# Kernel tuning notes

Measured on AMD Instinct MI355X. Metric: run time of the kernel, lower is better.

Reference implementation:

```python
import jax, jax.numpy as jnp
import numpy as np

B, N, S = 4, 8192, 2048
C1, C2 = 128, 256
CIN = C1 + C2  # 384
H1, H2 = 256, 256
BN_EPS = 1e-5


def setup_inputs() -> dict:
    key = jax.random.key(0)
    ks = jax.random.split(key, 12)
    inp = {
        "xyz1": jax.random.normal(ks[0], (B, N, 3), jnp.float32),
        "xyz2": jax.random.normal(ks[1], (B, S, 3), jnp.float32),
        "points1": jax.random.normal(ks[2], (B, C1, N), jnp.float32),
        "points2": jax.random.normal(ks[3], (B, C2, S), jnp.float32),
        # Conv1d(k=1) weights are [out, in]; BN affine params per channel
        "W1": jax.random.normal(ks[4], (H1, CIN), jnp.float32) * (1.0 / np.sqrt(CIN)),
        "b1": jnp.zeros((H1,), jnp.float32),
        "gamma1": jnp.ones((H1,), jnp.float32),
        "beta1": jnp.zeros((H1,), jnp.float32),
        "W2": jax.random.normal(ks[5], (H2, H1), jnp.float32) * (1.0 / np.sqrt(H1)),
        "b2": jnp.zeros((H2,), jnp.float32),
        "gamma2": jnp.ones((H2,), jnp.float32),
        "beta2": jnp.zeros((H2,), jnp.float32),
    }
    return inp


def _square_distance(src, dst):
    # src [B,N,3], dst [B,S,3] -> [B,N,S]
    d = -2.0 * jnp.einsum("bnc,bsc->bns", src, dst)
    d = d + jnp.sum(src * src, -1)[:, :, None]
    d = d + jnp.sum(dst * dst, -1)[:, None, :]
    return jnp.maximum(d, 0.0)


def _bn_relu(x, gamma, beta):
    # x [B,C,N]; BatchNorm1d in training mode: batch stats over (B, N), biased var
    mean = jnp.mean(x, axis=(0, 2), keepdims=True)
    var = jnp.mean((x - mean) ** 2, axis=(0, 2), keepdims=True)
    xhat = (x - mean) * jax.lax.rsqrt(var + BN_EPS)
    return jax.nn.relu(xhat * gamma[None, :, None] + beta[None, :, None])


def reference(xyz1, xyz2, points1, points2, W1, b1, gamma1, beta1, W2, b2, gamma2, beta2):
    dists = _square_distance(xyz1, xyz2)            # [B,N,S]
    neg_d, idx = jax.lax.top_k(-dists, 3)           # 3 smallest distances
    d3 = -neg_d                                     # [B,N,3]
    recip = 1.0 / (d3 + 1e-8)
    weight = recip / jnp.sum(recip, axis=2, keepdims=True)  # [B,N,3]
    pts2 = jnp.transpose(points2, (0, 2, 1))        # [B,S,C2]
    gathered = jax.vmap(lambda p, i: p[i])(pts2, idx)  # [B,N,3,C2]
    interp = jnp.einsum("bnkc,bnk->bcn", gathered, weight)  # [B,C2,N]
    new_pts = jnp.concatenate([points1, interp], axis=1)    # [B,CIN,N]
    x = jnp.einsum("oc,bcn->bon", W1, new_pts) + b1[None, :, None]
    x = _bn_relu(x, gamma1, beta1)
    x = jnp.einsum("oc,bcn->bon", W2, x) + b2[None, :, None]
    x = _bn_relu(x, gamma2, beta2)
    return x
```

## Files before the change

### kernel.cpp

```cpp
#include <hip/hip_runtime.h>

#define B_   4
#define N_   8192
#define S_   2048
#define C1_  128
#define C2_  256
#define CIN_ 384
#define H_   256

typedef short short8 __attribute__((ext_vector_type(8)));
typedef unsigned short ushort8 __attribute__((ext_vector_type(8)));
typedef float f32x4 __attribute__((ext_vector_type(4)));

__device__ __forceinline__ unsigned short f2bf(float x) {
  unsigned u = __float_as_uint(x);
  unsigned r = (u + 0x7fffu + ((u >> 16) & 1u)) >> 16;
  return (unsigned short)r;
}
__device__ __forceinline__ float bf2f(unsigned short h) {
  return __uint_as_float(((unsigned)h) << 16);
}
__device__ __forceinline__ void async16(const void* g, void* l) {
  __builtin_amdgcn_global_load_lds(
      (const __attribute__((address_space(1))) void*)g,
      (__attribute__((address_space(3))) void*)l, 16, 0, 0);
}

__global__ __launch_bounds__(256) void convw_kernel(const float* __restrict__ W1,
                                                    const float* __restrict__ W2,
                                                    unsigned short* __restrict__ W1b,
                                                    unsigned short* __restrict__ W2b) {
  int id = blockIdx.x * 256 + threadIdx.x;
  if (id < 98304) W1b[id] = f2bf(W1[id]);
  else            W2b[id - 98304] = f2bf(W2[id - 98304]);
}

__global__ __launch_bounds__(256) void transpose_kernel(
    const float* __restrict__ src, unsigned short* __restrict__ dst,
    int dstStride) {
  __shared__ float tile[64 * 65];
  const int b = blockIdx.z;
  const int n0 = blockIdx.x * 64;
  const int c0 = blockIdx.y * 64;
  const int C = gridDim.y * 64;
  const int Nsrc = gridDim.x * 64;
  const int tid = threadIdx.x;
  const float* sp = src + ((size_t)b * C + c0) * Nsrc;
  unsigned short* dp = dst + (size_t)b * Nsrc * dstStride;
  const int c_l = tid >> 2, nch = (tid & 3) * 16;
  const float* s = sp + (size_t)c_l * Nsrc + n0 + nch;
#pragma unroll
  for (int i = 0; i < 4; ++i)
    *(float4*)&tile[c_l * 65 + nch + i * 4] = *(const float4*)(s + i * 4);
  __syncthreads();
  const int n_l = tid >> 2, cch = (tid & 3) * 16;
  unsigned short pk[16];
#pragma unroll
  for (int i = 0; i < 16; ++i) pk[i] = f2bf(tile[(cch + i) * 65 + n_l]);
  unsigned short* d = dp + (size_t)(n0 + n_l) * dstStride + c0 + cch;
  *(uint4*)d = *(uint4*)pk;
  *(uint4*)(d + 8) = *(uint4*)(pk + 8);
}

__global__ __launch_bounds__(512) void knn_kernel(const float* __restrict__ xyz1,
                                                  const float* __restrict__ xyz2,
                                                  int* __restrict__ idx,
                                                  float* __restrict__ wgt) {
  __shared__ float4 t4[S_];
  __shared__ float kd[64][25];
  __shared__ int   ki[64][25];
  const int b  = blockIdx.x >> 7;
  const int n0 = (blockIdx.x & 127) << 6;
  const int tid = threadIdx.x;

  for (int i = tid; i < S_; i += 512) {
    float x = xyz2[(b * S_ + i) * 3 + 0];
    float y = xyz2[(b * S_ + i) * 3 + 1];
    float z = xyz2[(b * S_ + i) * 3 + 2];
    t4[i] = make_float4(-2.f * x, -2.f * y, -2.f * z,
                        fmaf(x, x, fmaf(y, y, z * z)));
  }
  __syncthreads();

  const int w = tid >> 6;
  const int ln = tid & 63;
  const int n = n0 + ln;
  const float px = xyz1[(b * N_ + n) * 3 + 0];
  const float py = xyz1[(b * N_ + n) * 3 + 1];
  const float pz = xyz1[(b * N_ + n) * 3 + 2];
  const float h = fmaf(px, px, fmaf(py, py, pz * pz));

  float d0 = 1e30f, d1 = 1e30f, d2 = 1e30f;
  int j0 = 0, j1 = 0, j2 = 0;
  const int jg0 = w * 256;
  const float4* tp = t4 + jg0;
#pragma unroll 4
  for (int j = 0; j < 256; ++j) {
    float4 t = tp[j];
    float d = fmaf(px, t.x, fmaf(py, t.y, fmaf(pz, t.z, t.w))) + h;
    d = fmaxf(d, 0.f);
    const int jj = jg0 + j;
    bool c0 = d < d0, c1 = d < d1, c2 = d < d2;
    float nd2 = c1 ? d1 : (c2 ? d : d2);
    int   nj2 = c1 ? j1 : (c2 ? jj : j2);
    float nd1 = c0 ? d0 : (c1 ? d : d1);
    int   nj1 = c0 ? j0 : (c1 ? jj : j1);
    d0 = c0 ? d : d0;
    j0 = c0 ? jj : j0;
    d1 = nd1; j1 = nj1;
    d2 = nd2; j2 = nj2;
  }
  kd[ln][w * 3 + 0] = d0; ki[ln][w * 3 + 0] = j0;
  kd[ln][w * 3 + 1] = d1; ki[ln][w * 3 + 1] = j1;
  kd[ln][w * 3 + 2] = d2; ki[ln][w * 3 + 2] = j2;
  __syncthreads();

  if (tid < 64) {
    float m0 = kd[tid][0], m1 = kd[tid][1], m2 = kd[tid][2];
    int   i0 = ki[tid][0], i1 = ki[tid][1], i2 = ki[tid][2];
#pragma unroll
    for (int s = 3; s < 24; ++s) {
      float d = kd[tid][s];
      int  jj = ki[tid][s];
      bool c0 = d < m0, c1 = d < m1, c2 = d < m2;
      float nd2 = c1 ? m1 : (c2 ? d : m2);
      int   nj2 = c1 ? i1 : (c2 ? jj : i2);
      float nd1 = c0 ? m0 : (c1 ? d : m1);
      int   nj1 = c0 ? i0 : (c1 ? jj : i1);
      m0 = c0 ? d : m0;
      i0 = c0 ? jj : i0;
      m1 = nd1; i1 = nj1;
      m2 = nd2; i2 = nj2;
    }
    float r0 = 1.f / (m0 + 1e-8f);
    float r1 = 1.f / (m1 + 1e-8f);
    float r2 = 1.f / (m2 + 1e-8f);
    float rs = 1.f / (r0 + r1 + r2);
    int base = (b * N_ + n0 + tid) * 3;
    idx[base + 0] = i0;
    idx[base + 1] = i1;
    idx[base + 2] = i2;
    wgt[base + 0] = r0 * rs;
    wgt[base + 1] = r1 * rs;
    wgt[base + 2] = r2 * rs;
  }
}

__global__ __launch_bounds__(256) void interp_gather_kernel(
    const unsigned short* __restrict__ p2t, const int* __restrict__ idx,
    const float* __restrict__ wgt, unsigned short* __restrict__ Xt) {
  const int w = threadIdx.x >> 6, lane = threadIdx.x & 63;
  const int gbase = blockIdx.x * 128 + w * 32;
#pragma unroll 2
  for (int i = 0; i < 32; ++i) {
    const int gn = gbase + i;
    const int b = gn >> 13;
    const int base = gn * 3;
    int i0 = idx[base], i1 = idx[base + 1], i2 = idx[base + 2];
    float w0 = wgt[base], w1 = wgt[base + 1], w2 = wgt[base + 2];
    const unsigned short* r0 = p2t + (((size_t)(b * S_ + i0)) << 8) + lane * 4;
    const unsigned short* r1 = p2t + (((size_t)(b * S_ + i1)) << 8) + lane * 4;
    const unsigned short* r2 = p2t + (((size_t)(b * S_ + i2)) << 8) + lane * 4;
    uint2 a = *(const uint2*)r0;
    uint2 c = *(const uint2*)r1;
    uint2 e = *(const uint2*)r2;
    const unsigned short* ap = (const unsigned short*)&a;
    const unsigned short* cp = (const unsigned short*)&c;
    const unsigned short* ep = (const unsigned short*)&e;
    unsigned short pk[4];
#pragma unroll
    for (int k = 0; k < 4; ++k) {
      float v = w0 * bf2f(ap[k]) + w1 * bf2f(cp[k]) + w2 * bf2f(ep[k]);
      pk[k] = f2bf(v);
    }
    *(uint2*)(Xt + (size_t)gn * CIN_ + C1_ + lane * 4) = *(uint2*)pk;
  }
}

template <int K, bool FUSE>
__global__ __launch_bounds__(256, 2) void gemm_mfma_kernel(
    const unsigned short* __restrict__ Wb,
    const unsigned short* __restrict__ Bmat,
    const float* __restrict__ bias,
    const float* __restrict__ bnscale, const float* __restrict__ bnshift,
    float* __restrict__ OutF, unsigned short* __restrict__ OutB,
    float* __restrict__ Psum, float* __restrict__ Psq) {
  __shared__ __align__(16) short Als[128 * 32];
  __shared__ __align__(16) short Bls[128 * 32];
  const int tid = threadIdx.x;
  const int lane = tid & 63;
  const int col = lane & 15, quad = lane >> 4;
  const int wid = tid >> 6;
  const int wr = wid >> 1, wc = wid & 1;
  const int nBase = blockIdx.x * 128;
  const int oBase = blockIdx.y * 128;
  const int b = blockIdx.z;

  f32x4 acc[4][4];
#pragma unroll
  for (int i = 0; i < 4; ++i)
#pragma unroll
    for (int j = 0; j < 4; ++j) acc[i][j] = (f32x4){0.f, 0.f, 0.f, 0.f};

  const int f0 = tid * 16;
  const int m0 = f0 >> 6;
  const int kb0 = f0 & 63;
  const char* Abase = (const char*)Wb;
  const char* Bbase = (const char*)Bmat;
  char* AldsW = (char*)Als + (tid & ~63) * 16;
  char* BldsW = (char*)Bls + (tid & ~63) * 16;

  for (int k0 = 0; k0 < K; k0 += 32) {
    __syncthreads();
    async16(Abase + ((size_t)(oBase + m0) * K + k0) * 2 + kb0, AldsW);
    async16(Abase + ((size_t)(oBase + m0 + 64) * K + k0) * 2 + kb0, AldsW + 4096);
    if (!FUSE) {
      async16(Bbase + ((size_t)(b * N_ + nBase + m0) * K + k0) * 2 + kb0, BldsW);
      async16(Bbase + ((size_t)(b * N_ + nBase + m0 + 64) * K + k0) * 2 + kb0,
              BldsW + 4096);
    } else {
#pragma unroll
      for (int r = 0; r < 2; ++r) {
        const int f = f0 + r * 4096;
        const int n = f >> 6;
        const int kb = f & 63;
        const int ke = k0 + (kb >> 1);
        ushort8 h = *(const ushort8*)(Bbase +
            ((size_t)(b * N_ + nBase + n) * K + k0) * 2 + kb);
        float4 s0 = *(const float4*)(bnscale + ke);
        float4 s1 = *(const float4*)(bnscale + ke + 4);
        float4 t0 = *(const float4*)(bnshift + ke);
        float4 t1 = *(const float4*)(bnshift + ke + 4);
        float sc[8] = {s0.x, s0.y, s0.z, s0.w, s1.x, s1.y, s1.z, s1.w};
        float sh[8] = {t0.x, t0.y, t0.z, t0.w, t1.x, t1.y, t1.z, t1.w};
        unsigned short pk[8];
#pragma unroll
        for (int e = 0; e < 8; ++e)
          pk[e] = f2bf(fmaxf(fmaf(bf2f(h[e]), sc[e], sh[e]), 0.f));
        *(uint4*)((char*)Bls + f) = *(uint4*)pk;
      }
    }
    __syncthreads();
    short8 af[4], bfr[4];
#pragma unroll
    for (int i = 0; i < 4; ++i)
      af[i] = *(const short8*)(Als + (wr * 64 + i * 16 + col) * 32 + quad * 8);
#pragma unroll
    for (int j = 0; j < 4; ++j)
      bfr[j] = *(const short8*)(Bls + (wc * 64 + j * 16 + col) * 32 + quad * 8);
#pragma unroll
    for (int i = 0; i < 4; ++i)
#pragma unroll
      for (int j = 0; j < 4; ++j)
        acc[i][j] = __builtin_amdgcn_mfma_f32_16x16x32_bf16(af[i], bfr[j],
                                                            acc[i][j], 0, 0, 0);
  }

  float s_acc[4][4], q_acc[4][4];
#pragma unroll
  for (int i = 0; i < 4; ++i) {
    const int oloc = wr * 64 + i * 16 + quad * 4;
    float4 bb = *(const float4*)(bias + oBase + oloc);
    float s[4] = {0.f, 0.f, 0.f, 0.f}, q[4] = {0.f, 0.f, 0.f, 0.f};
#pragma unroll
    for (int j = 0; j < 4; ++j) {
      const int n = nBase + wc * 64 + j * 16 + col;
      float v0 = acc[i][j][0] + bb.x;
      float v1 = acc[i][j][1] + bb.y;
      float v2 = acc[i][j][2] + bb.z;
      float v3 = acc[i][j][3] + bb.w;
      if (!FUSE) {
        unsigned short pk[4] = {f2bf(v0), f2bf(v1), f2bf(v2), f2bf(v3)};
        *(uint2*)(OutB + (size_t)(b * N_ + n) * H_ + oBase + oloc) = *(uint2*)pk;
      } else {
        float* op = OutF + ((size_t)b * H_ + oBase + oloc) * N_ + n;
        op[0] = v0; op[N_] = v1; op[2 * N_] = v2; op[3 * N_] = v3;
      }
      s[0] += v0; q[0] = fmaf(v0, v0, q[0]);
      s[1] += v1; q[1] = fmaf(v1, v1, q[1]);
      s[2] += v2; q[2] = fmaf(v2, v2, q[2]);
      s[3] += v3; q[3] = fmaf(v3, v3, q[3]);
    }
#pragma unroll
    for (int reg = 0; reg < 4; ++reg) {
      float ss = s[reg], qq = q[reg];
#pragma unroll
      for (int m = 1; m < 16; m <<= 1) {
        ss += __shfl_xor(ss, m);
        qq += __shfl_xor(qq, m);
      }
      s_acc[i][reg] = ss;
      q_acc[i][reg] = qq;
    }
  }
  __syncthreads();
  float* red = (float*)Als;
#pragma unroll
  for (int i = 0; i < 4; ++i)
#pragma unroll
    for (int reg = 0; reg < 4; ++reg)
      if (col == 0) {
        int ch = wr * 64 + i * 16 + quad * 4 + reg;
        red[wc * 256 + ch] = s_acc[i][reg];
        red[wc * 256 + 128 + ch] = q_acc[i][reg];
      }
  __syncthreads();
  {
    const int wcb = tid >> 7, ch = tid & 127;
    const int part = (blockIdx.z * 64 + blockIdx.x) * 2 + wcb;
    Psum[part * 256 + oBase + ch] = red[wcb * 256 + ch];
    Psq[part * 256 + oBase + ch]  = red[wcb * 256 + 128 + ch];
  }
}

__global__ __launch_bounds__(1024) void finalize_bn_kernel(
    const float* __restrict__ Psum, const float* __restrict__ Psq,
    const float* __restrict__ gamma, const float* __restrict__ beta,
    float* __restrict__ scale, float* __restrict__ shift) {
  __shared__ float ls[4][2][256];
  const int tid = threadIdx.x;
  const int g = tid >> 8, ch = tid & 255;
  float s = 0.f, q = 0.f;
#pragma unroll 4
  for (int p = g * 128; p < (g + 1) * 128; ++p) {
    s += Psum[p * 256 + ch];
    q += Psq[p * 256 + ch];
  }
  ls[g][0][ch] = s;
  ls[g][1][ch] = q;
  __syncthreads();
  if (tid < 256) {
    float ss = ls[0][0][ch] + ls[1][0][ch] + ls[2][0][ch] + ls[3][0][ch];
    float qq = ls[0][1][ch] + ls[1][1][ch] + ls[2][1][ch] + ls[3][1][ch];
    const float inv_n = 1.f / 32768.f;
    float mean = ss * inv_n;
    float var = qq * inv_n - mean * mean;
    float sc = gamma[ch] * rsqrtf(var + 1e-5f);
    scale[ch] = sc;
    shift[ch] = fmaf(-mean, sc, beta[ch]);
  }
}

__global__ __launch_bounds__(256) void bn_apply_kernel(float* __restrict__ io,
                                                       const float* __restrict__ scale,
                                                       const float* __restrict__ shift) {
  int id = blockIdx.x * 256 + threadIdx.x;
  int row = id >> 11;
  int o = row & 255;
  float sc = scale[o], sh = shift[o];
  float4 v = ((float4*)io)[id];
  v.x = fmaxf(fmaf(v.x, sc, sh), 0.f);
  v.y = fmaxf(fmaf(v.y, sc, sh), 0.f);
  v.z = fmaxf(fmaf(v.z, sc, sh), 0.f);
  v.w = fmaxf(fmaf(v.w, sc, sh), 0.f);
  ((float4*)io)[id] = v;
}

extern "C" void kernel_launch(void* const* d_in, const int* in_sizes, int n_in,
                              void* d_out, int out_size, void* d_ws, size_t ws_size,
                              hipStream_t stream) {
  const float* xyz1 = (const float*)d_in[0];
  const float* xyz2 = (const float*)d_in[1];
  const float* p1   = (const float*)d_in[2];
  const float* p2   = (const float*)d_in[3];
  const float* W1   = (const float*)d_in[4];
  const float* b1   = (const float*)d_in[5];
  const float* g1   = (const float*)d_in[6];
  const float* be1  = (const float*)d_in[7];
  const float* W2   = (const float*)d_in[8];
  const float* b2   = (const float*)d_in[9];
  const float* g2   = (const float*)d_in[10];
  const float* be2  = (const float*)d_in[11];
  float* out = (float*)d_out;

  unsigned short* ws = (unsigned short*)d_ws;
  unsigned short* Xt  = ws;
  unsigned short* Y1t = Xt + 12582912;
  unsigned short* p2t = Y1t + 8388608;
  unsigned short* W1b = p2t + 2097152;
  unsigned short* W2b = W1b + 98304;
  float* wgt   = (float*)(W2b + 65536);
  int*   idxb  = (int*)(wgt + 98304);
  float* Psum1 = (float*)(idxb + 98304);
  float* Psq1  = Psum1 + 131072;
  float* Psum2 = Psq1 + 131072;
  float* Psq2  = Psum2 + 131072;
  float* scale1 = Psq2 + 131072;
  float* shift1 = scale1 + 256;
  float* scale2 = shift1 + 256;
  float* shift2 = scale2 + 256;

  convw_kernel<<<640, 256, 0, stream>>>(W1, W2, W1b, W2b);
  transpose_kernel<<<dim3(32, 4, 4), 256, 0, stream>>>(p2, p2t, C2_);
  knn_kernel<<<512, 512, 0, stream>>>(xyz1, xyz2, idxb, wgt);
  transpose_kernel<<<dim3(128, 2, 4), 256, 0, stream>>>(p1, Xt, CIN_);
  interp_gather_kernel<<<256, 256, 0, stream>>>(p2t, idxb, wgt, Xt);

  dim3 gg(64, 2, 4);
  gemm_mfma_kernel<CIN_, false><<<gg, 256, 0, stream>>>(
      W1b, Xt, b1, nullptr, nullptr, nullptr, Y1t, Psum1, Psq1);
  finalize_bn_kernel<<<1, 1024, 0, stream>>>(Psum1, Psq1, g1, be1, scale1, shift1);
  gemm_mfma_kernel<H_, true><<<gg, 256, 0, stream>>>(
      W2b, Y1t, b2, scale1, shift1, out, nullptr, Psum2, Psq2);
  finalize_bn_kernel<<<1, 1024, 0, stream>>>(Psum2, Psq2, g2, be2, scale2, shift2);
  bn_apply_kernel<<<8192, 256, 0, stream>>>(out, scale2, shift2);
}
```

Before: 220.6 us.

## Merge prep stages into one kernel and run GEMM/BN chain as cooperative megakernel

Converts weights, transposes both point feature tensors, and runs KNN inside a single block-partitioned prep kernel; the KNN part now uses 256-thread blocks scanning 512 candidates per wave. The interpolation gather, both GEMMs, BN statistics finalization and the final BN+ReLU run in one cooperative kernel with grid syncs, keeping the second GEMM's accumulators in registers so the output is written once instead of written then re-read by a separate apply pass. This targets launch overhead and the extra full-output round trip, at the cost of grid-wide barriers, finalize steps done by only 8 blocks while the rest idle, and a fallback path if cooperative launch fails.

```diff
diff --git a/kernel.cpp b/kernel.cpp
--- a/kernel.cpp
+++ b/kernel.cpp
@@ -1,4 +1,7 @@
 #include <hip/hip_runtime.h>
+#include <hip/hip_cooperative_groups.h>
+
+namespace cg = cooperative_groups;
 
 #define B_   4
 #define N_   8192
@@ -26,27 +29,21 @@
       (__attribute__((address_space(3))) void*)l, 16, 0, 0);
 }
 
-__global__ __launch_bounds__(256) void convw_kernel(const float* __restrict__ W1,
-                                                    const float* __restrict__ W2,
-                                                    unsigned short* __restrict__ W1b,
-                                                    unsigned short* __restrict__ W2b) {
-  int id = blockIdx.x * 256 + threadIdx.x;
-  if (id < 98304) W1b[id] = f2bf(W1[id]);
-  else            W2b[id - 98304] = f2bf(W2[id - 98304]);
-}
-
-__global__ __launch_bounds__(256) void transpose_kernel(
+union PrepShared {
+  struct {
+    float4 t4[S_];
+    float  kd[64][13];
+    int    ki[64][13];
+  } k;
+  float tile[64 * 65];
+};
+
+__device__ __forceinline__ void transpose_tile(
     const float* __restrict__ src, unsigned short* __restrict__ dst,
-    int dstStride) {
-  __shared__ float tile[64 * 65];
-  const int b = blockIdx.z;
-  const int n0 = blockIdx.x * 64;
-  const int c0 = blockIdx.y * 64;
-  const int C = gridDim.y * 64;
-  const int Nsrc = gridDim.x * 64;
-  const int tid = threadIdx.x;
-  const float* sp = src + ((size_t)b * C + c0) * Nsrc;
-  unsigned short* dp = dst + (size_t)b * Nsrc * dstStride;
+    float* tile, int x, int y, int z, int C, int Nsrc, int dstStride, int tid) {
+  const int n0 = x * 64, c0 = y * 64;
+  const float* sp = src + ((size_t)z * C + c0) * Nsrc;
+  unsigned short* dp = dst + (size_t)z * Nsrc * dstStride;
   const int c_l = tid >> 2, nch = (tid & 3) * 16;
   const float* s = sp + (size_t)c_l * Nsrc + n0 + nch;
 #pragma unroll
@@ -62,87 +59,109 @@
   *(uint4*)(d + 8) = *(uint4*)(pk + 8);
 }
 
-__global__ __launch_bounds__(512) void knn_kernel(const float* __restrict__ xyz1,
-                                                  const float* __restrict__ xyz2,
-                                                  int* __restrict__ idx,
-                                                  float* __restrict__ wgt) {
-  __shared__ float4 t4[S_];
-  __shared__ float kd[64][25];
-  __shared__ int   ki[64][25];
-  const int b  = blockIdx.x >> 7;
-  const int n0 = (blockIdx.x & 127) << 6;
-  const int tid = threadIdx.x;
-
-  for (int i = tid; i < S_; i += 512) {
-    float x = xyz2[(b * S_ + i) * 3 + 0];
-    float y = xyz2[(b * S_ + i) * 3 + 1];
-    float z = xyz2[(b * S_ + i) * 3 + 2];
-    t4[i] = make_float4(-2.f * x, -2.f * y, -2.f * z,
-                        fmaf(x, x, fmaf(y, y, z * z)));
-  }
-  __syncthreads();
-
-  const int w = tid >> 6;
-  const int ln = tid & 63;
-  const int n = n0 + ln;
-  const float px = xyz1[(b * N_ + n) * 3 + 0];
-  const float py = xyz1[(b * N_ + n) * 3 + 1];
-  const float pz = xyz1[(b * N_ + n) * 3 + 2];
-  const float h = fmaf(px, px, fmaf(py, py, pz * pz));
-
-  float d0 = 1e30f, d1 = 1e30f, d2 = 1e30f;
-  int j0 = 0, j1 = 0, j2 = 0;
-  const int jg0 = w * 256;
-  const float4* tp = t4 + jg0;
+__global__ __launch_bounds__(256) void prep_kernel(
+    const float* __restrict__ W1, const float* __restrict__ W2,
+    unsigned short* __restrict__ W1b, unsigned short* __restrict__ W2b,
+    const float* __restrict__ p1, const float* __restrict__ p2,
+    unsigned short* __restrict__ Xt, unsigned short* __restrict__ p2t,
+    const float* __restrict__ xyz1, const float* __restrict__ xyz2,
+    int* __restrict__ idx, float* __restrict__ wgt) {
+  __shared__ PrepShared sm;
+  const int blk = blockIdx.x, tid = threadIdx.x;
+
+  if (blk < 640) {
+    int id = blk * 256 + tid;
+    if (id < 98304) W1b[id] = f2bf(W1[id]);
+    else            W2b[id - 98304] = f2bf(W2[id - 98304]);
+    return;
+  }
+  if (blk < 1152) {
+    int t = blk - 640;
+    transpose_tile(p2, p2t, sm.tile, t & 31, (t >> 5) & 3, t >> 7,
+                   C2_, S_, C2_, tid);
+    return;
+  }
+  if (blk < 2176) {
+    int t = blk - 1152;
+    transpose_tile(p1, Xt, sm.tile, t & 127, (t >> 7) & 1, t >> 8,
+                   C1_, N_, CIN_, tid);
+    return;
+  }
+  {
+    const int t = blk - 2176;
+    const int b = t >> 7;
+    const int n0 = (t & 127) << 6;
+    for (int i = tid; i < S_; i += 256) {
+      float x = xyz2[(b * S_ + i) * 3 + 0];
+      float y = xyz2[(b * S_ + i) * 3 + 1];
+      float z = xyz2[(b * S_ + i) * 3 + 2];
+      sm.k.t4[i] = make_float4(-2.f * x, -2.f * y, -2.f * z,
+                               fmaf(x, x, fmaf(y, y, z * z)));
+    }
+    __syncthreads();
+
+    const int w = tid >> 6;
+    const int ln = tid & 63;
+    const int n = n0 + ln;
+    const float px = xyz1[(b * N_ + n) * 3 + 0];
+    const float py = xyz1[(b * N_ + n) * 3 + 1];
+    const float pz = xyz1[(b * N_ + n) * 3 + 2];
+    const float h = fmaf(px, px, fmaf(py, py, pz * pz));
+
+    float d0 = 1e30f, d1 = 1e30f, d2 = 1e30f;
+    int j0 = 0, j1 = 0, j2 = 0;
+    const int jg0 = w * 512;
+    const float4* tp = sm.k.t4 + jg0;
 #pragma unroll 4
-  for (int j = 0; j < 256; ++j) {
-    float4 t = tp[j];
-    float d = fmaf(px, t.x, fmaf(py, t.y, fmaf(pz, t.z, t.w))) + h;
-    d = fmaxf(d, 0.f);
-    const int jj = jg0 + j;
-    bool c0 = d < d0, c1 = d < d1, c2 = d < d2;
-    float nd2 = c1 ? d1 : (c2 ? d : d2);
-    int   nj2 = c1 ? j1 : (c2 ? jj : j2);
-    float nd1 = c0 ? d0 : (c1 ? d : d1);
-    int   nj1 = c0 ? j0 : (c1 ? jj : j1);
-    d0 = c0 ? d : d0;
-    j0 = c0 ? jj : j0;
-    d1 = nd1; j1 = nj1;
-    d2 = nd2; j2 = nj2;
-  }
-  kd[ln][w * 3 + 0] = d0; ki[ln][w * 3 + 0] = j0;
-  kd[ln][w * 3 + 1] = d1; ki[ln][w * 3 + 1] = j1;
-  kd[ln][w * 3 + 2] = d2; ki[ln][w * 3 + 2] = j2;
-  __syncthreads();
-
-  if (tid < 64) {
-    float m0 = kd[tid][0], m1 = kd[tid][1], m2 = kd[tid][2];
-    int   i0 = ki[tid][0], i1 = ki[tid][1], i2 = ki[tid][2];
-#pragma unroll
-    for (int s = 3; s < 24; ++s) {
-      float d = kd[tid][s];
-      int  jj = ki[tid][s];
-      bool c0 = d < m0, c1 = d < m1, c2 = d < m2;
-      float nd2 = c1 ? m1 : (c2 ? d : m2);
-      int   nj2 = c1 ? i1 : (c2 ? jj : i2);
-      float nd1 = c0 ? m0 : (c1 ? d : m1);
-      int   nj1 = c0 ? i0 : (c1 ? jj : i1);
-      m0 = c0 ? d : m0;
-      i0 = c0 ? jj : i0;
-      m1 = nd1; i1 = nj1;
-      m2 = nd2; i2 = nj2;
-    }
-    float r0 = 1.f / (m0 + 1e-8f);
-    float r1 = 1.f / (m1 + 1e-8f);
-    float r2 = 1.f / (m2 + 1e-8f);
-    float rs = 1.f / (r0 + r1 + r2);
-    int base = (b * N_ + n0 + tid) * 3;
-    idx[base + 0] = i0;
-    idx[base + 1] = i1;
-    idx[base + 2] = i2;
-    wgt[base + 0] = r0 * rs;
-    wgt[base + 1] = r1 * rs;
-    wgt[base + 2] = r2 * rs;
+    for (int j = 0; j < 512; ++j) {
+      float4 tt = tp[j];
+      float d = fmaf(px, tt.x, fmaf(py, tt.y, fmaf(pz, tt.z, tt.w))) + h;
+      d = fmaxf(d, 0.f);
+      const int jj = jg0 + j;
+      bool c0 = d < d0, c1 = d < d1, c2 = d < d2;
+      float nd2 = c1 ? d1 : (c2 ? d : d2);
+      int   nj2 = c1 ? j1 : (c2 ? jj : j2);
+      float nd1 = c0 ? d0 : (c1 ? d : d1);
+      int   nj1 = c0 ? j0 : (c1 ? jj : j1);
+      d0 = c0 ? d : d0;
+      j0 = c0 ? jj : j0;
+      d1 = nd1; j1 = nj1;
+      d2 = nd2; j2 = nj2;
+    }
+    sm.k.kd[ln][w * 3 + 0] = d0; sm.k.ki[ln][w * 3 + 0] = j0;
+    sm.k.kd[ln][w * 3 + 1] = d1; sm.k.ki[ln][w * 3 + 1] = j1;
+    sm.k.kd[ln][w * 3 + 2] = d2; sm.k.ki[ln][w * 3 + 2] = j2;
+    __syncthreads();
+
+    if (tid < 64) {
+      float m0 = sm.k.kd[tid][0], m1 = sm.k.kd[tid][1], m2 = sm.k.kd[tid][2];
+      int   i0 = sm.k.ki[tid][0], i1 = sm.k.ki[tid][1], i2 = sm.k.ki[tid][2];
+#pragma unroll
+      for (int s = 3; s < 12; ++s) {
+        float d = sm.k.kd[tid][s];
+        int  jj = sm.k.ki[tid][s];
+        bool c0 = d < m0, c1 = d < m1, c2 = d < m2;
+        float nd2 = c1 ? m1 : (c2 ? d : m2);
+        int   nj2 = c1 ? i1 : (c2 ? jj : i2);
+        float nd1 = c0 ? m0 : (c1 ? d : m1);
+        int   nj1 = c0 ? i0 : (c1 ? jj : i1);
+        m0 = c0 ? d : m0;
+        i0 = c0 ? jj : i0;
+        m1 = nd1; i1 = nj1;
+        m2 = nd2; i2 = nj2;
+      }
+      float r0 = 1.f / (m0 + 1e-8f);
+      float r1 = 1.f / (m1 + 1e-8f);
+      float r2 = 1.f / (m2 + 1e-8f);
+      float rs = 1.f / (r0 + r1 + r2);
+      int base = (b * N_ + n0 + tid) * 3;
+      idx[base + 0] = i0;
+      idx[base + 1] = i1;
+      idx[base + 2] = i2;
+      wgt[base + 0] = r0 * rs;
+      wgt[base + 1] = r1 * rs;
+      wgt[base + 2] = r2 * rs;
+    }
   }
 }
 
@@ -150,20 +169,17 @@
     const unsigned short* __restrict__ p2t, const int* __restrict__ idx,
     const float* __restrict__ wgt, unsigned short* __restrict__ Xt) {
   const int w = threadIdx.x >> 6, lane = threadIdx.x & 63;
-  const int gbase = blockIdx.x * 128 + w * 32;
+  const int gbase = blockIdx.x * 64 + w * 16;
 #pragma unroll 2
-  for (int i = 0; i < 32; ++i) {
+  for (int i = 0; i < 16; ++i) {
     const int gn = gbase + i;
     const int b = gn >> 13;
     const int base = gn * 3;
     int i0 = idx[base], i1 = idx[base + 1], i2 = idx[base + 2];
     float w0 = wgt[base], w1 = wgt[base + 1], w2 = wgt[base + 2];
-    const unsigned short* r0 = p2t + (((size_t)(b * S_ + i0)) << 8) + lane * 4;
-    const unsigned short* r1 = p2t + (((size_t)(b * S_ + i1)) << 8) + lane * 4;
-    const unsigned short* r2 = p2t + (((size_t)(b * S_ + i2)) << 8) + lane * 4;
-    uint2 a = *(const uint2*)r0;
-    uint2 c = *(const uint2*)r1;
-    uint2 e = *(const uint2*)r2;
+    uint2 a = *(const uint2*)(p2t + (((size_t)(b * S_ + i0)) << 8) + lane * 4);
+    uint2 c = *(const uint2*)(p2t + (((size_t)(b * S_ + i1)) << 8) + lane * 4);
+    uint2 e = *(const uint2*)(p2t + (((size_t)(b * S_ + i2)) << 8) + lane * 4);
     const unsigned short* ap = (const unsigned short*)&a;
     const unsigned short* cp = (const unsigned short*)&c;
     const unsigned short* ep = (const unsigned short*)&e;
@@ -356,6 +372,266 @@
   ((float4*)io)[id] = v;
 }
 
+struct MegaArgs {
+  const unsigned short* p2t;
+  const int* idx;
+  const float* wgt;
+  unsigned short* Xt;
+  const unsigned short* W1b;
+  const float *b1, *g1, *be1;
+  const unsigned short* W2b;
+  const float *b2, *g2, *be2;
+  unsigned short* Y1t;
+  float *Psum1, *Psq1, *Psum2, *Psq2;
+  float *scale1, *shift1, *scale2, *shift2;
+  float* out;
+};
+
+template <int K, bool FUSE, bool WRITE_OUT>
+__device__ __forceinline__ void gemm_phase(
+    const unsigned short* __restrict__ Wb,
+    const unsigned short* __restrict__ Bmat,
+    const float* __restrict__ bias,
+    const float* __restrict__ bnscale, const float* __restrict__ bnshift,
+    unsigned short* __restrict__ OutB,
+    float* __restrict__ Psum, float* __restrict__ Psq,
+    short* Als, short* Bls, f32x4 (&acc)[4][4],
+    const int tid, const int nBase, const int oBase, const int b,
+    const int part2) {
+  const int lane = tid & 63;
+  const int col = lane & 15, quad = lane >> 4;
+  const int wid = tid >> 6;
+  const int wr = wid >> 1, wc = wid & 1;
+
+#pragma unroll
+  for (int i = 0; i < 4; ++i)
+#pragma unroll
+    for (int j = 0; j < 4; ++j) acc[i][j] = (f32x4){0.f, 0.f, 0.f, 0.f};
+
+  const int f0 = tid * 16;
+  const int m0 = f0 >> 6;
+  const int kb0 = f0 & 63;
+  const char* Abase = (const char*)Wb;
+  const char* Bbase = (const char*)Bmat;
+  char* AldsW = (char*)Als + (tid & ~63) * 16;
+  char* BldsW = (char*)Bls + (tid & ~63) * 16;
+
+  for (int k0 = 0; k0 < K; k0 += 32) {
+    __syncthreads();
+    async16(Abase + ((size_t)(oBase + m0) * K + k0) * 2 + kb0, AldsW);
+    async16(Abase + ((size_t)(oBase + m0 + 64) * K + k0) * 2 + kb0, AldsW + 4096);
+    if (!FUSE) {
+      async16(Bbase + ((size_t)(b * N_ + nBase + m0) * K + k0) * 2 + kb0, BldsW);
+      async16(Bbase + ((size_t)(b * N_ + nBase + m0 + 64) * K + k0) * 2 + kb0,
+              BldsW + 4096);
+    } else {
+#pragma unroll
+      for (int r = 0; r < 2; ++r) {
+        const int f = f0 + r * 4096;
+        const int n = f >> 6;
+        const int kb = f & 63;
+        const int ke = k0 + (kb >> 1);
+        ushort8 h = *(const ushort8*)(Bbase +
+            ((size_t)(b * N_ + nBase + n) * K + k0) * 2 + kb);
+        float4 s0 = *(const float4*)(bnscale + ke);
+        float4 s1 = *(const float4*)(bnscale + ke + 4);
+        float4 t0 = *(const float4*)(bnshift + ke);
+        float4 t1 = *(const float4*)(bnshift + ke + 4);
+        float sc[8] = {s0.x, s0.y, s0.z, s0.w, s1.x, s1.y, s1.z, s1.w};
+        float sh[8] = {t0.x, t0.y, t0.z, t0.w, t1.x, t1.y, t1.z, t1.w};
+        unsigned short pk[8];
+#pragma unroll
+        for (int e = 0; e < 8; ++e)
+          pk[e] = f2bf(fmaxf(fmaf(bf2f(h[e]), sc[e], sh[e]), 0.f));
+        *(uint4*)((char*)Bls + f) = *(uint4*)pk;
+      }
+    }
+    __syncthreads();
+    short8 af[4], bfr[4];
+#pragma unroll
+    for (int i = 0; i < 4; ++i)
+      af[i] = *(const short8*)(Als + (wr * 64 + i * 16 + col) * 32 + quad * 8);
+#pragma unroll
+    for (int j = 0; j < 4; ++j)
+      bfr[j] = *(const short8*)(Bls + (wc * 64 + j * 16 + col) * 32 + quad * 8);
+#pragma unroll
+    for (int i = 0; i < 4; ++i)
+#pragma unroll
+      for (int j = 0; j < 4; ++j)
+        acc[i][j] = __builtin_amdgcn_mfma_f32_16x16x32_bf16(af[i], bfr[j],
+                                                            acc[i][j], 0, 0, 0);
+  }
+
+  float s_acc[4][4], q_acc[4][4];
+#pragma unroll
+  for (int i = 0; i < 4; ++i) {
+    const int oloc = wr * 64 + i * 16 + quad * 4;
+    float4 bb = *(const float4*)(bias + oBase + oloc);
+    float s[4] = {0.f, 0.f, 0.f, 0.f}, q[4] = {0.f, 0.f, 0.f, 0.f};
+#pragma unroll
+    for (int j = 0; j < 4; ++j) {
+      const int n = nBase + wc * 64 + j * 16 + col;
+      float v0 = acc[i][j][0] + bb.x;
+      float v1 = acc[i][j][1] + bb.y;
+      float v2 = acc[i][j][2] + bb.z;
+      float v3 = acc[i][j][3] + bb.w;
+      if (WRITE_OUT) {
+        unsigned short pk[4] = {f2bf(v0), f2bf(v1), f2bf(v2), f2bf(v3)};
+        *(uint2*)(OutB + (size_t)(b * N_ + n) * H_ + oBase + oloc) = *(uint2*)pk;
+      }
+      s[0] += v0; q[0] = fmaf(v0, v0, q[0]);
+      s[1] += v1; q[1] = fmaf(v1, v1, q[1]);
+      s[2] += v2; q[2] = fmaf(v2, v2, q[2]);
+      s[3] += v3; q[3] = fmaf(v3, v3, q[3]);
+    }
+#pragma unroll
+    for (int reg = 0; reg < 4; ++reg) {
+      float ss = s[reg], qq = q[reg];
+#pragma unroll
+      for (int m = 1; m < 16; m <<= 1) {
+        ss += __shfl_xor(ss, m);
+        qq += __shfl_xor(qq, m);
+      }
+      s_acc[i][reg] = ss;
+      q_acc[i][reg] = qq;
+    }
+  }
+  __syncthreads();
+  float* red = (float*)Als;
+#pragma unroll
+  for (int i = 0; i < 4; ++i)
+#pragma unroll
+    for (int reg = 0; reg < 4; ++reg)
+      if (col == 0) {
+        int ch = wr * 64 + i * 16 + quad * 4 + reg;
+        red[wc * 256 + ch] = s_acc[i][reg];
+        red[wc * 256 + 128 + ch] = q_acc[i][reg];
+      }
+  __syncthreads();
+  {
+    const int wcb = tid >> 7, ch = tid & 127;
+    const int part = part2 * 2 + wcb;
+    Psum[part * 256 + oBase + ch] = red[wcb * 256 + ch];
+    Psq[part * 256 + oBase + ch]  = red[wcb * 256 + 128 + ch];
+  }
+  __syncthreads();
+}
+
+__device__ __forceinline__ void finalize_bn_dev(
+    const float* __restrict__ Psum, const float* __restrict__ Psq,
+    const float* __restrict__ gamma, const float* __restrict__ beta,
+    float* __restrict__ scale, float* __restrict__ shift,
+    int blk, int tid) {
+  const int ch = blk * 32 + (tid >> 3);
+  const int sl = tid & 7;
+  float s = 0.f, q = 0.f;
+#pragma unroll 4
+  for (int p = sl * 64; p < sl * 64 + 64; ++p) {
+    s += Psum[p * 256 + ch];
+    q += Psq[p * 256 + ch];
+  }
+#pragma unroll
+  for (int m = 1; m < 8; m <<= 1) {
+    s += __shfl_xor(s, m);
+    q += __shfl_xor(q, m);
+  }
+  if (sl == 0) {
+    const float inv_n = 1.f / 32768.f;
+    float mean = s * inv_n;
+    float var = q * inv_n - mean * mean;
+    float sc = gamma[ch] * rsqrtf(var + 1e-5f);
+    scale[ch] = sc;
+    shift[ch] = fmaf(-mean, sc, beta[ch]);
+  }
+}
+
+__global__ __launch_bounds__(256, 2) void mega_kernel(MegaArgs a) {
+  __shared__ __align__(16) short Als[128 * 32];
+  __shared__ __align__(16) short Bls[128 * 32];
+  const int tid = threadIdx.x;
+  const int blk = blockIdx.x;
+  const int nb = blk & 63, ob = (blk >> 6) & 1, b = blk >> 7;
+  const int nBase = nb * 128, oBase = ob * 128;
+  cg::grid_group grid = cg::this_grid();
+
+  {
+    const int w = tid >> 6, lane = tid & 63;
+    const int gn0 = blk * 64 + w * 16;
+#pragma unroll 2
+    for (int i = 0; i < 16; ++i) {
+      const int gn = gn0 + i;
+      const int bb = gn >> 13;
+      const int base = gn * 3;
+      int i0 = a.idx[base], i1 = a.idx[base + 1], i2 = a.idx[base + 2];
+      float w0 = a.wgt[base], w1 = a.wgt[base + 1], w2 = a.wgt[base + 2];
+      uint2 x = *(const uint2*)(a.p2t + (((size_t)(bb * S_ + i0)) << 8) + lane * 4);
+      uint2 y = *(const uint2*)(a.p2t + (((size_t)(bb * S_ + i1)) << 8) + lane * 4);
+      uint2 z = *(const uint2*)(a.p2t + (((size_t)(bb * S_ + i2)) << 8) + lane * 4);
+      const unsigned short* xp = (const unsigned short*)&x;
+      const unsigned short* yp = (const unsigned short*)&y;
+      const unsigned short* zp = (const unsigned short*)&z;
+      unsigned short pk[4];
+#pragma unroll
+      for (int k = 0; k < 4; ++k) {
+        float v = w0 * bf2f(xp[k]) + w1 * bf2f(yp[k]) + w2 * bf2f(zp[k]);
+        pk[k] = f2bf(v);
+      }
+      *(uint2*)(a.Xt + (size_t)gn * CIN_ + C1_ + lane * 4) = *(uint2*)pk;
+    }
+  }
+  __threadfence();
+  grid.sync();
+
+  f32x4 acc[4][4];
+
+  gemm_phase<CIN_, false, true>(a.W1b, a.Xt, a.b1, nullptr, nullptr,
+                                a.Y1t, a.Psum1, a.Psq1, Als, Bls, acc,
+                                tid, nBase, oBase, b, b * 64 + nb);
+  __threadfence();
+  grid.sync();
+
+  if (blk < 8) finalize_bn_dev(a.Psum1, a.Psq1, a.g1, a.be1, a.scale1, a.shift1, blk, tid);
+  __threadfence();
+  grid.sync();
+
+  gemm_phase<H_, true, false>(a.W2b, a.Y1t, a.b2, a.scale1, a.shift1,
+                              nullptr, a.Psum2, a.Psq2, Als, Bls, acc,
+                              tid, nBase, oBase, b, b * 64 + nb);
+  __threadfence();
+  grid.sync();
+
+  if (blk < 8) finalize_bn_dev(a.Psum2, a.Psq2, a.g2, a.be2, a.scale2, a.shift2, blk, tid);
+  __threadfence();
+  grid.sync();
+
+  {
+    const int lane = tid & 63;
+    const int col = lane & 15, quad = lane >> 4;
+    const int wid = tid >> 6;
+    const int wr = wid >> 1, wc = wid & 1;
+#pragma unroll
+    for (int i = 0; i < 4; ++i) {
+      const int o = oBase + wr * 64 + i * 16 + quad * 4;
+      float4 sc = *(const float4*)(a.scale2 + o);
+      float4 sh = *(const float4*)(a.shift2 + o);
+      float4 bb = *(const float4*)(a.b2 + o);
+      sh.x = fmaf(sc.x, bb.x, sh.x);
+      sh.y = fmaf(sc.y, bb.y, sh.y);
+      sh.z = fmaf(sc.z, bb.z, sh.z);
+      sh.w = fmaf(sc.w, bb.w, sh.w);
+#pragma unroll
+      for (int j = 0; j < 4; ++j) {
+        const int n = nBase + wc * 64 + j * 16 + col;
+        float* op = a.out + ((size_t)b * H_ + o) * N_ + n;
+        op[0]      = fmaxf(fmaf(acc[i][j][0], sc.x, sh.x), 0.f);
+        op[N_]     = fmaxf(fmaf(acc[i][j][1], sc.y, sh.y), 0.f);
+        op[2 * N_] = fmaxf(fmaf(acc[i][j][2], sc.z, sh.z), 0.f);
+        op[3 * N_] = fmaxf(fmaf(acc[i][j][3], sc.w, sh.w), 0.f);
+      }
+    }
+  }
+}
+
 extern "C" void kernel_launch(void* const* d_in, const int* in_sizes, int n_in,
                               void* d_out, int out_size, void* d_ws, size_t ws_size,
                               hipStream_t stream) {
@@ -390,18 +666,30 @@
   float* scale2 = shift1 + 256;
   float* shift2 = scale2 + 256;
 
-  convw_kernel<<<640, 256, 0, stream>>>(W1, W2, W1b, W2b);
-  transpose_kernel<<<dim3(32, 4, 4), 256, 0, stream>>>(p2, p2t, C2_);
-  knn_kernel<<<512, 512, 0, stream>>>(xyz1, xyz2, idxb, wgt);
-  transpose_kernel<<<dim3(128, 2, 4), 256, 0, stream>>>(p1, Xt, CIN_);
-  interp_gather_kernel<<<256, 256, 0, stream>>>(p2t, idxb, wgt, Xt);
-
-  dim3 gg(64, 2, 4);
-  gemm_mfma_kernel<CIN_, false><<<gg, 256, 0, stream>>>(
-      W1b, Xt, b1, nullptr, nullptr, nullptr, Y1t, Psum1, Psq1);
-  finalize_bn_kernel<<<1, 1024, 0, stream>>>(Psum1, Psq1, g1, be1, scale1, shift1);
-  gemm_mfma_kernel<H_, true><<<gg, 256, 0, stream>>>(
-      W2b, Y1t, b2, scale1, shift1, out, nullptr, Psum2, Psq2);
-  finalize_bn_kernel<<<1, 1024, 0, stream>>>(Psum2, Psq2, g2, be2, scale2, shift2);
-  bn_apply_kernel<<<8192, 256, 0, stream>>>(out, scale2, shift2);
-}
+  prep_kernel<<<2688, 256, 0, stream>>>(W1, W2, W1b, W2b, p1, p2, Xt, p2t,
+                                        xyz1, xyz2, idxb, wgt);
+
+  MegaArgs ma;
+  ma.p2t = p2t; ma.idx = idxb; ma.wgt = wgt; ma.Xt = Xt;
+  ma.W1b = W1b; ma.b1 = b1; ma.g1 = g1; ma.be1 = be1;
+  ma.W2b = W2b; ma.b2 = b2; ma.g2 = g2; ma.be2 = be2;
+  ma.Y1t = Y1t;
+  ma.Psum1 = Psum1; ma.Psq1 = Psq1; ma.Psum2 = Psum2; ma.Psq2 = Psq2;
+  ma.scale1 = scale1; ma.shift1 = shift1; ma.scale2 = scale2; ma.shift2 = shift2;
+  ma.out = out;
+  void* kargs[] = {&ma};
+  hipError_t cerr = hipLaunchCooperativeKernel(mega_kernel, dim3(512), dim3(256),
+                                               kargs, 0, stream);
+  if (cerr != hipSuccess) {
+    (void)hipGetLastError();
+    interp_gather_kernel<<<512, 256, 0, stream>>>(p2t, idxb, wgt, Xt);
+    dim3 gg(64, 2, 4);
+    gemm_mfma_kernel<CIN_, false><<<gg, 256, 0, stream>>>(
+        W1b, Xt, b1, nullptr, nullptr, nullptr, Y1t, Psum1, Psq1);
+    finalize_bn_kernel<<<1, 1024, 0, stream>>>(Psum1, Psq1, g1, be1, scale1, shift1);
+    gemm_mfma_kernel<H_, true><<<gg, 256, 0, stream>>>(
+        W2b, Y1t, b2, scale1, shift1, out, nullptr, Psum2, Psq2);
+    finalize_bn_kernel<<<1, 1024, 0, stream>>>(Psum2, Psq2, g2, be2, scale2, shift2);
+    bn_apply_kernel<<<8192, 256, 0, stream>>>(out, scale2, shift2);
+  }
+}
```

Result: slower. 700.9 us (+217.7%).

## Merge prep kernels into one launch and fuse KNN with interpolation gather

Applied to the files above, without the earlier changes.

Three preprocessing launches (weight cast, two transposes) are merged into one prep kernel that dispatches on block index. The KNN kernel now performs the interpolation gather itself, keeping indices and weights in shared memory instead of writing them to global memory for a separate kernel. The KNN block is cut from 512 to 256 threads, so each wave scans 512 candidates instead of 256. This lowers the parallelism of the distance scan per block in exchange for fewer launches and less global traffic.

```diff
diff --git a/kernel.cpp b/kernel.cpp
--- a/kernel.cpp
+++ b/kernel.cpp
@@ -26,27 +26,12 @@
       (__attribute__((address_space(3))) void*)l, 16, 0, 0);
 }
 
-__global__ __launch_bounds__(256) void convw_kernel(const float* __restrict__ W1,
-                                                    const float* __restrict__ W2,
-                                                    unsigned short* __restrict__ W1b,
-                                                    unsigned short* __restrict__ W2b) {
-  int id = blockIdx.x * 256 + threadIdx.x;
-  if (id < 98304) W1b[id] = f2bf(W1[id]);
-  else            W2b[id - 98304] = f2bf(W2[id - 98304]);
-}
-
-__global__ __launch_bounds__(256) void transpose_kernel(
+__device__ __forceinline__ void transpose_tile(
     const float* __restrict__ src, unsigned short* __restrict__ dst,
-    int dstStride) {
-  __shared__ float tile[64 * 65];
-  const int b = blockIdx.z;
-  const int n0 = blockIdx.x * 64;
-  const int c0 = blockIdx.y * 64;
-  const int C = gridDim.y * 64;
-  const int Nsrc = gridDim.x * 64;
-  const int tid = threadIdx.x;
-  const float* sp = src + ((size_t)b * C + c0) * Nsrc;
-  unsigned short* dp = dst + (size_t)b * Nsrc * dstStride;
+    float* tile, int x, int y, int z, int C, int Nsrc, int dstStride, int tid) {
+  const int n0 = x * 64, c0 = y * 64;
+  const float* sp = src + ((size_t)z * C + c0) * Nsrc;
+  unsigned short* dp = dst + (size_t)z * Nsrc * dstStride;
   const int c_l = tid >> 2, nch = (tid & 3) * 16;
   const float* s = sp + (size_t)c_l * Nsrc + n0 + nch;
 #pragma unroll
@@ -62,18 +47,47 @@
   *(uint4*)(d + 8) = *(uint4*)(pk + 8);
 }
 
-__global__ __launch_bounds__(512) void knn_kernel(const float* __restrict__ xyz1,
-                                                  const float* __restrict__ xyz2,
-                                                  int* __restrict__ idx,
-                                                  float* __restrict__ wgt) {
+__global__ __launch_bounds__(256) void prep_kernel(
+    const float* __restrict__ W1, const float* __restrict__ W2,
+    unsigned short* __restrict__ W1b, unsigned short* __restrict__ W2b,
+    const float* __restrict__ p1, const float* __restrict__ p2,
+    unsigned short* __restrict__ Xt, unsigned short* __restrict__ p2t) {
+  __shared__ float tile[64 * 65];
+  const int blk = blockIdx.x, tid = threadIdx.x;
+
+  if (blk < 640) {
+    int id = blk * 256 + tid;
+    if (id < 98304) W1b[id] = f2bf(W1[id]);
+    else            W2b[id - 98304] = f2bf(W2[id - 98304]);
+    return;
+  }
+  if (blk < 1152) {
+    int t = blk - 640;
+    transpose_tile(p2, p2t, tile, t & 31, (t >> 5) & 3, t >> 7,
+                   C2_, S_, C2_, tid);
+    return;
+  }
+  {
+    int t = blk - 1152;
+    transpose_tile(p1, Xt, tile, t & 127, (t >> 7) & 1, t >> 8,
+                   C1_, N_, CIN_, tid);
+  }
+}
+
+__global__ __launch_bounds__(256) void knn_interp_kernel(
+    const float* __restrict__ xyz1, const float* __restrict__ xyz2,
+    const unsigned short* __restrict__ p2t, unsigned short* __restrict__ Xt) {
   __shared__ float4 t4[S_];
-  __shared__ float kd[64][25];
-  __shared__ int   ki[64][25];
-  const int b  = blockIdx.x >> 7;
-  const int n0 = (blockIdx.x & 127) << 6;
+  __shared__ float kd[64][13];
+  __shared__ int   ki[64][13];
+  __shared__ int   sidx[64][3];
+  __shared__ float swgt[64][3];
+  const int blk = blockIdx.x;
+  const int b  = blk >> 7;
+  const int n0 = (blk & 127) << 6;
   const int tid = threadIdx.x;
 
-  for (int i = tid; i < S_; i += 512) {
+  for (int i = tid; i < S_; i += 256) {
     float x = xyz2[(b * S_ + i) * 3 + 0];
     float y = xyz2[(b * S_ + i) * 3 + 1];
     float z = xyz2[(b * S_ + i) * 3 + 2];
@@ -82,44 +96,46 @@
   }
   __syncthreads();
 
-  const int w = tid >> 6;
-  const int ln = tid & 63;
-  const int n = n0 + ln;
-  const float px = xyz1[(b * N_ + n) * 3 + 0];
-  const float py = xyz1[(b * N_ + n) * 3 + 1];
-  const float pz = xyz1[(b * N_ + n) * 3 + 2];
-  const float h = fmaf(px, px, fmaf(py, py, pz * pz));
-
-  float d0 = 1e30f, d1 = 1e30f, d2 = 1e30f;
-  int j0 = 0, j1 = 0, j2 = 0;
-  const int jg0 = w * 256;
-  const float4* tp = t4 + jg0;
+  {
+    const int w = tid >> 6;
+    const int ln = tid & 63;
+    const int n = n0 + ln;
+    const float px = xyz1[(b * N_ + n) * 3 + 0];
+    const float py = xyz1[(b * N_ + n) * 3 + 1];
+    const float pz = xyz1[(b * N_ + n) * 3 + 2];
+    const float h = fmaf(px, px, fmaf(py, py, pz * pz));
+
+    float d0 = 1e30f, d1 = 1e30f, d2 = 1e30f;
+    int j0 = 0, j1 = 0, j2 = 0;
+    const int jg0 = w * 512;
+    const float4* tp = t4 + jg0;
 #pragma unroll 4
-  for (int j = 0; j < 256; ++j) {
-    float4 t = tp[j];
-    float d = fmaf(px, t.x, fmaf(py, t.y, fmaf(pz, t.z, t.w))) + h;
-    d = fmaxf(d, 0.f);
-    const int jj = jg0 + j;
-    bool c0 = d < d0, c1 = d < d1, c2 = d < d2;
-    float nd2 = c1 ? d1 : (c2 ? d : d2);
-    int   nj2 = c1 ? j1 : (c2 ? jj : j2);
-    float nd1 = c0 ? d0 : (c1 ? d : d1);
-    int   nj1 = c0 ? j0 : (c1 ? jj : j1);
-    d0 = c0 ? d : d0;
-    j0 = c0 ? jj : j0;
-    d1 = nd1; j1 = nj1;
-    d2 = nd2; j2 = nj2;
-  }
-  kd[ln][w * 3 + 0] = d0; ki[ln][w * 3 + 0] = j0;
-  kd[ln][w * 3 + 1] = d1; ki[ln][w * 3 + 1] = j1;
-  kd[ln][w * 3 + 2] = d2; ki[ln][w * 3 + 2] = j2;
+    for (int j = 0; j < 512; ++j) {
+      float4 tt = tp[j];
+      float d = fmaf(px, tt.x, fmaf(py, tt.y, fmaf(pz, tt.z, tt.w))) + h;
+      d = fmaxf(d, 0.f);
+      const int jj = jg0 + j;
+      bool c0 = d < d0, c1 = d < d1, c2 = d < d2;
+      float nd2 = c1 ? d1 : (c2 ? d : d2);
+      int   nj2 = c1 ? j1 : (c2 ? jj : j2);
+      float nd1 = c0 ? d0 : (c1 ? d : d1);
+      int   nj1 = c0 ? j0 : (c1 ? jj : j1);
+      d0 = c0 ? d : d0;
+      j0 = c0 ? jj : j0;
+      d1 = nd1; j1 = nj1;
+      d2 = nd2; j2 = nj2;
+    }
+    kd[ln][w * 3 + 0] = d0; ki[ln][w * 3 + 0] = j0;
+    kd[ln][w * 3 + 1] = d1; ki[ln][w * 3 + 1] = j1;
+    kd[ln][w * 3 + 2] = d2; ki[ln][w * 3 + 2] = j2;
+  }
   __syncthreads();
 
   if (tid < 64) {
     float m0 = kd[tid][0], m1 = kd[tid][1], m2 = kd[tid][2];
     int   i0 = ki[tid][0], i1 = ki[tid][1], i2 = ki[tid][2];
 #pragma unroll
-    for (int s = 3; s < 24; ++s) {
+    for (int s = 3; s < 12; ++s) {
       float d = kd[tid][s];
       int  jj = ki[tid][s];
       bool c0 = d < m0, c1 = d < m1, c2 = d < m2;
@@ -136,44 +152,33 @@
     float r1 = 1.f / (m1 + 1e-8f);
     float r2 = 1.f / (m2 + 1e-8f);
     float rs = 1.f / (r0 + r1 + r2);
-    int base = (b * N_ + n0 + tid) * 3;
-    idx[base + 0] = i0;
-    idx[base + 1] = i1;
-    idx[base + 2] = i2;
-    wgt[base + 0] = r0 * rs;
-    wgt[base + 1] = r1 * rs;
-    wgt[base + 2] = r2 * rs;
-  }
-}
-
-__global__ __launch_bounds__(256) void interp_gather_kernel(
-    const unsigned short* __restrict__ p2t, const int* __restrict__ idx,
-    const float* __restrict__ wgt, unsigned short* __restrict__ Xt) {
-  const int w = threadIdx.x >> 6, lane = threadIdx.x & 63;
-  const int gbase = blockIdx.x * 128 + w * 32;
+    sidx[tid][0] = i0; sidx[tid][1] = i1; sidx[tid][2] = i2;
+    swgt[tid][0] = r0 * rs; swgt[tid][1] = r1 * rs; swgt[tid][2] = r2 * rs;
+  }
+  __syncthreads();
+
+  {
+    const int w = tid >> 6, lane = tid & 63;
 #pragma unroll 2
-  for (int i = 0; i < 32; ++i) {
-    const int gn = gbase + i;
-    const int b = gn >> 13;
-    const int base = gn * 3;
-    int i0 = idx[base], i1 = idx[base + 1], i2 = idx[base + 2];
-    float w0 = wgt[base], w1 = wgt[base + 1], w2 = wgt[base + 2];
-    const unsigned short* r0 = p2t + (((size_t)(b * S_ + i0)) << 8) + lane * 4;
-    const unsigned short* r1 = p2t + (((size_t)(b * S_ + i1)) << 8) + lane * 4;
-    const unsigned short* r2 = p2t + (((size_t)(b * S_ + i2)) << 8) + lane * 4;
-    uint2 a = *(const uint2*)r0;
-    uint2 c = *(const uint2*)r1;
-    uint2 e = *(const uint2*)r2;
-    const unsigned short* ap = (const unsigned short*)&a;
-    const unsigned short* cp = (const unsigned short*)&c;
-    const unsigned short* ep = (const unsigned short*)&e;
-    unsigned short pk[4];
-#pragma unroll
-    for (int k = 0; k < 4; ++k) {
-      float v = w0 * bf2f(ap[k]) + w1 * bf2f(cp[k]) + w2 * bf2f(ep[k]);
-      pk[k] = f2bf(v);
-    }
-    *(uint2*)(Xt + (size_t)gn * CIN_ + C1_ + lane * 4) = *(uint2*)pk;
+    for (int i = 0; i < 16; ++i) {
+      const int q = w * 16 + i;
+      const int gn = b * N_ + n0 + q;
+      int i0 = sidx[q][0], i1 = sidx[q][1], i2 = sidx[q][2];
+      float w0 = swgt[q][0], w1 = swgt[q][1], w2 = swgt[q][2];
+      uint2 x = *(const uint2*)(p2t + (((size_t)(b * S_ + i0)) << 8) + lane * 4);
+      uint2 y = *(const uint2*)(p2t + (((size_t)(b * S_ + i1)) << 8) + lane * 4);
+      uint2 z = *(const uint2*)(p2t + (((size_t)(b * S_ + i2)) << 8) + lane * 4);
+      const unsigned short* xp = (const unsigned short*)&x;
+      const unsigned short* yp = (const unsigned short*)&y;
+      const unsigned short* zp = (const unsigned short*)&z;
+      unsigned short pk[4];
+#pragma unroll
+      for (int k = 0; k < 4; ++k) {
+        float v = w0 * bf2f(xp[k]) + w1 * bf2f(yp[k]) + w2 * bf2f(zp[k]);
+        pk[k] = f2bf(v);
+      }
+      *(uint2*)(Xt + (size_t)gn * CIN_ + C1_ + lane * 4) = *(uint2*)pk;
+    }
   }
 }
 
@@ -379,9 +384,7 @@
   unsigned short* p2t = Y1t + 8388608;
   unsigned short* W1b = p2t + 2097152;
   unsigned short* W2b = W1b + 98304;
-  float* wgt   = (float*)(W2b + 65536);
-  int*   idxb  = (int*)(wgt + 98304);
-  float* Psum1 = (float*)(idxb + 98304);
+  float* Psum1 = (float*)(W2b + 65536);
   float* Psq1  = Psum1 + 131072;
   float* Psum2 = Psq1 + 131072;
   float* Psq2  = Psum2 + 131072;
@@ -390,11 +393,8 @@
   float* scale2 = shift1 + 256;
   float* shift2 = scale2 + 256;
 
-  convw_kernel<<<640, 256, 0, stream>>>(W1, W2, W1b, W2b);
-  transpose_kernel<<<dim3(32, 4, 4), 256, 0, stream>>>(p2, p2t, C2_);
-  knn_kernel<<<512, 512, 0, stream>>>(xyz1, xyz2, idxb, wgt);
-  transpose_kernel<<<dim3(128, 2, 4), 256, 0, stream>>>(p1, Xt, CIN_);
-  interp_gather_kernel<<<256, 256, 0, stream>>>(p2t, idxb, wgt, Xt);
+  prep_kernel<<<2176, 256, 0, stream>>>(W1, W2, W1b, W2b, p1, p2, Xt, p2t);
+  knn_interp_kernel<<<512, 256, 0, stream>>>(xyz1, xyz2, p2t, Xt);
 
   dim3 gg(64, 2, 4);
   gemm_mfma_kernel<CIN_, false><<<gg, 256, 0, stream>>>(
```

Result: faster. 212.7 us (-3.6%).
